# Performance work log

Hardware: AMD Instinct MI355X
Metric: run time of the kernel (lower is better)

## Reference

```python
import jax, jax.numpy as jnp
import numpy as np

B, S, D, H, C = 2, 2048, 1024, 16, 64

def setup_inputs() -> dict:
    key = jax.random.key(0)
    kx, kq, kk, kv, ko = jax.random.split(key, 5)
    scale = 0.02
    return {
        "x": jax.random.normal(kx, (B, S, D), dtype=jnp.float32),
        "Wq": jax.random.normal(kq, (D, H, C), dtype=jnp.float32) * scale,
        "Wk": jax.random.normal(kk, (D, H, C), dtype=jnp.float32) * scale,
        "Wv": jax.random.normal(kv, (D, H, C), dtype=jnp.float32) * scale,
        "Wo": jax.random.normal(ko, (H, C, D), dtype=jnp.float32) * scale,
    }

def reference(x, Wq, Wk, Wv, Wo):
    # project to per-head q/k/v: [B,S,H,C]
    q = jnp.einsum('bqd,dhc->bqhc', x, Wq)
    k = jnp.einsum('bkd,dhc->bkhc', x, Wk)
    v = jnp.einsum('bkd,dhc->bkhc', x, Wv)
    q = q * (C ** -0.5)
    alphas = jnp.einsum('bqhc,bkhc->bhqk', q, k)  # [B,H,S,S]
    weights = jax.nn.softmax(alphas, axis=-1)
    out = jnp.einsum('bhqk,bkhc->bqhc', weights, v)
    return jnp.einsum('bqhc,hcd->bqd', out, Wo)
```

## Files before the change

### kernel.cpp

```cpp
#include <hip/hip_runtime.h>
#include <hip/hip_bf16.h>
#include <stdint.h>
#include <stddef.h>

typedef __bf16 bf16;
typedef __bf16 bf16x4 __attribute__((ext_vector_type(4)));
typedef __bf16 bf16x8 __attribute__((ext_vector_type(8)));
typedef float f32x4 __attribute__((ext_vector_type(4)));

#define DEV __device__ __forceinline__

DEV void async16(const bf16* g, bf16* l) {
    __builtin_amdgcn_global_load_lds(
        (const __attribute__((address_space(1))) void*)g,
        (__attribute__((address_space(3))) void*)l,
        16, 0, 0);
}


__global__ void convert_x(const float* __restrict__ in, bf16* __restrict__ out, int n) {
    int i = (blockIdx.x * blockDim.x + threadIdx.x) * 4;
    if (i >= n) return;
    const float4 v = *(const float4*)(in + i);
    bf16 o4[4] = {(bf16)v.x, (bf16)v.y, (bf16)v.z, (bf16)v.w};
    *(uint2*)(out + i) = *(const uint2*)o4;
}

__global__ void transpose_cvt_all(const float* __restrict__ Wq, const float* __restrict__ Wk,
                                  const float* __restrict__ Wv, const float* __restrict__ Wo,
                                  bf16* __restrict__ WqkvT, bf16* __restrict__ WoT) {
    const float* src;
    bf16* dst;
    float scale = 1.0f;
    switch (blockIdx.z) {
        case 0: src = Wq; dst = WqkvT; scale = 0.125f * 1.4426950408889634f; break;
        case 1: src = Wk; dst = WqkvT + 1024 * 1024; break;
        case 2: src = Wv; dst = WqkvT + 2 * 1024 * 1024; break;
        default: src = Wo; dst = WoT; break;
    }
    __shared__ float t[32][33];
    const int c0 = blockIdx.x * 32, r0 = blockIdx.y * 32;
    const int tx = threadIdx.x & 31, ty = threadIdx.x >> 5;
#pragma unroll
    for (int i = 0; i < 32; i += 8)
        t[ty + i][tx] = src[(size_t)(r0 + ty + i) * 1024 + c0 + tx];
    __syncthreads();
#pragma unroll
    for (int i = 0; i < 32; i += 8)
        dst[(size_t)(c0 + ty + i) * 1024 + r0 + tx] = (bf16)(t[tx][ty + i] * scale);
}

__global__ void transpose_v(const bf16* __restrict__ V, bf16* __restrict__ VT) {
    __shared__ bf16 t[32][33];
    const int c0 = blockIdx.x * 32, r0 = blockIdx.y * 32;
    const int tx = threadIdx.x & 31, ty = threadIdx.x >> 5;
#pragma unroll
    for (int i = 0; i < 32; i += 8)
        t[ty + i][tx] = V[(size_t)(r0 + ty + i) * 3072 + c0 + tx];
    __syncthreads();
#pragma unroll
    for (int i = 0; i < 32; i += 8)
        VT[(size_t)(c0 + ty + i) * 4096 + r0 + tx] = t[tx][ty + i];
}


template <bool OUT_F32>
__global__ __launch_bounds__(256, 3) void gemm_bt(
    const bf16* __restrict__ A, const bf16* __restrict__ BT, void* __restrict__ Cout,
    int M, int N, int K) {
    __shared__ __attribute__((aligned(16))) bf16 As[2 * 128 * 32];
    __shared__ __attribute__((aligned(16))) bf16 Bs[2 * 128 * 32];
    const int tid = threadIdx.x;
    const int wid = tid >> 6;
    const int lane = tid & 63;
    const int quad = lane >> 4;
    const int l16 = lane & 15;
    const int wm = wid >> 1, wn = wid & 1;
    const int m0 = blockIdx.y * 128, n0 = blockIdx.x * 128;

    const int srow = wid * 32 + (lane >> 2);
    const int skcol = (lane & 3) * 8;
    const bf16* ag = A + (size_t)(m0 + srow) * K + skcol;
    const bf16* bg = BT + (size_t)(n0 + srow) * K + skcol;

    f32x4 acc[4][4];
#pragma unroll
    for (int i = 0; i < 4; ++i)
#pragma unroll
        for (int j = 0; j < 4; ++j) acc[i][j] = (f32x4){0.f, 0.f, 0.f, 0.f};

    for (int k0 = 0; k0 < K; k0 += 64) {
#pragma unroll
        for (int p = 0; p < 2; ++p) {
            async16(ag + k0 + p * 32, &As[p * 4096 + (wid * 32) * 32]);
            async16(ag + (size_t)16 * K + k0 + p * 32, &As[p * 4096 + (wid * 32 + 16) * 32]);
            async16(bg + k0 + p * 32, &Bs[p * 4096 + (wid * 32) * 32]);
            async16(bg + (size_t)16 * K + k0 + p * 32, &Bs[p * 4096 + (wid * 32 + 16) * 32]);
        }
        __syncthreads();

#pragma unroll
        for (int ks = 0; ks < 2; ++ks) {
            bf16x8 af[4], bfr[4];
#pragma unroll
            for (int mi = 0; mi < 4; ++mi)
                af[mi] = *(const bf16x8*)&As[ks * 4096 + (wm * 64 + mi * 16 + l16) * 32 + quad * 8];
#pragma unroll
            for (int ni = 0; ni < 4; ++ni)
                bfr[ni] = *(const bf16x8*)&Bs[ks * 4096 + (wn * 64 + ni * 16 + l16) * 32 + quad * 8];
#pragma unroll
            for (int mi = 0; mi < 4; ++mi)
#pragma unroll
                for (int ni = 0; ni < 4; ++ni)
                    acc[mi][ni] = __builtin_amdgcn_mfma_f32_16x16x32_bf16(
                        af[mi], bfr[ni], acc[mi][ni], 0, 0, 0);
        }
        __syncthreads();
    }

    if (OUT_F32) {
        float* C = (float*)Cout;
#pragma unroll
        for (int mi = 0; mi < 4; ++mi)
#pragma unroll
            for (int ni = 0; ni < 4; ++ni)
#pragma unroll
                for (int r = 0; r < 4; ++r)
                    C[(size_t)(m0 + wm * 64 + mi * 16 + quad * 4 + r) * N +
                      (n0 + wn * 64 + ni * 16 + l16)] = acc[mi][ni][r];
    } else {
        bf16* C = (bf16*)Cout;
#pragma unroll
        for (int mi = 0; mi < 4; ++mi)
#pragma unroll
            for (int ni = 0; ni < 4; ++ni)
#pragma unroll
                for (int r = 0; r < 4; ++r)
                    C[(size_t)(m0 + wm * 64 + mi * 16 + quad * 4 + r) * N +
                      (n0 + wn * 64 + ni * 16 + l16)] = (bf16)acc[mi][ni][r];
    }
}


__global__ __launch_bounds__(256, 2) void flash_attn(
    const bf16* __restrict__ QKV, const bf16* __restrict__ VT, bf16* __restrict__ att) {
    __shared__ float Osc[2][32 * 256];
    __shared__ float Lred[4][128];
    __shared__ float Linv[128];

    const int tid = threadIdx.x, wid = tid >> 6, lane = tid & 63;
    const int quad = lane >> 4, l16 = lane & 15;
    const int qt = blockIdx.x;
    const int bh = blockIdx.y;
    const int b = bh >> 4, h = bh & 15;
    const int q0 = qt * 128;

    bf16x8 qf[8][2];
    {
        const bf16* qbase = QKV + (size_t)(b * 2048 + q0 + l16) * 3072 + h * 64 + quad * 8;
#pragma unroll
        for (int mi = 0; mi < 8; ++mi)
#pragma unroll
            for (int ks = 0; ks < 2; ++ks)
                qf[mi][ks] = *(const bf16x8*)(qbase + (size_t)mi * 16 * 3072 + ks * 32);
    }

    const bf16* kbase = QKV + (size_t)(b * 2048 + wid * 16 + l16) * 3072 + 1024 + h * 64 + quad * 8;
    const bf16* vbase = VT + (size_t)(h * 64 + l16) * 4096 + b * 2048 + wid * 16 + quad * 4;

    f32x4 o[8][4];
#pragma unroll
    for (int mi = 0; mi < 8; ++mi)
#pragma unroll
        for (int ct = 0; ct < 4; ++ct) o[mi][ct] = (f32x4){0.f, 0.f, 0.f, 0.f};
    float lsum[8];
#pragma unroll
    for (int mi = 0; mi < 8; ++mi) lsum[mi] = 0.f;

    for (int kc = 0; kc < 32; ++kc) {
        const bf16* kp = kbase + (size_t)kc * 64 * 3072;
        const bf16x8 kf0 = *(const bf16x8*)(kp);
        const bf16x8 kf1 = *(const bf16x8*)(kp + 32);

        const bf16* vp = vbase + kc * 64;
        bf16x8 vf[4];
#pragma unroll
        for (int ct = 0; ct < 4; ++ct) {
            const bf16x4 t = *(const bf16x4*)(vp + (size_t)ct * 16 * 4096);
            vf[ct] = (bf16x8){t[0], t[1], t[2], t[3],
                              (bf16)0.f, (bf16)0.f, (bf16)0.f, (bf16)0.f};
        }

#pragma unroll
        for (int mi = 0; mi < 8; ++mi) {
            f32x4 s = (f32x4){0.f, 0.f, 0.f, 0.f};
            s = __builtin_amdgcn_mfma_f32_16x16x32_bf16(kf0, qf[mi][0], s, 0, 0, 0);
            s = __builtin_amdgcn_mfma_f32_16x16x32_bf16(kf1, qf[mi][1], s, 0, 0, 0);

            const float p0 = __builtin_amdgcn_exp2f(s[0]);
            const float p1 = __builtin_amdgcn_exp2f(s[1]);
            const float p2 = __builtin_amdgcn_exp2f(s[2]);
            const float p3 = __builtin_amdgcn_exp2f(s[3]);
            lsum[mi] += (p0 + p1) + (p2 + p3);
            const bf16x8 pf = (bf16x8){(bf16)p0, (bf16)p1, (bf16)p2, (bf16)p3,
                                       (bf16)0.f, (bf16)0.f, (bf16)0.f, (bf16)0.f};
#pragma unroll
            for (int ct = 0; ct < 4; ++ct)
                o[mi][ct] = __builtin_amdgcn_mfma_f32_16x16x32_bf16(pf, vf[ct], o[mi][ct], 0, 0, 0);
        }
    }

#pragma unroll
    for (int mi = 0; mi < 8; ++mi) {
        lsum[mi] += __shfl_xor(lsum[mi], 16);
        lsum[mi] += __shfl_xor(lsum[mi], 32);
    }
    if (quad == 0) {
#pragma unroll
        for (int mi = 0; mi < 8; ++mi) Lred[wid][mi * 16 + l16] = lsum[mi];
    }
    if (wid >= 2) {
        float* dst = &Osc[wid - 2][0];
#pragma unroll
        for (int mi = 0; mi < 8; ++mi)
#pragma unroll
            for (int ct = 0; ct < 4; ++ct)
                *(f32x4*)(dst + (mi * 4 + ct) * 256 + lane * 4) = o[mi][ct];
    }
    __syncthreads();

    if (tid < 128) {
        const float l = Lred[0][tid] + Lred[1][tid] + Lred[2][tid] + Lred[3][tid];
        Linv[tid] = 1.0f / l;
    }
    if (wid < 2) {
        const float* src = &Osc[wid][0];
#pragma unroll
        for (int mi = 0; mi < 8; ++mi)
#pragma unroll
            for (int ct = 0; ct < 4; ++ct)
                o[mi][ct] += *(const f32x4*)(src + (mi * 4 + ct) * 256 + lane * 4);
    }
    __syncthreads();

    if (wid == 1) {
        float* dst = &Osc[0][0];
#pragma unroll
        for (int mi = 0; mi < 8; ++mi)
#pragma unroll
            for (int ct = 0; ct < 4; ++ct)
                *(f32x4*)(dst + (mi * 4 + ct) * 256 + lane * 4) = o[mi][ct];
    }
    __syncthreads();

    if (wid == 0) {
        const float* src = &Osc[0][0];
#pragma unroll
        for (int mi = 0; mi < 8; ++mi)
#pragma unroll
            for (int ct = 0; ct < 4; ++ct)
                o[mi][ct] += *(const f32x4*)(src + (mi * 4 + ct) * 256 + lane * 4);
#pragma unroll
        for (int mi = 0; mi < 8; ++mi)
#pragma unroll
            for (int r = 0; r < 4; ++r) {
                const float inv = Linv[mi * 16 + quad * 4 + r];
                bf16* orow = att + (size_t)(b * 2048 + q0 + mi * 16 + quad * 4 + r) * 1024 + h * 64 + l16;
#pragma unroll
                for (int ct = 0; ct < 4; ++ct)
                    orow[ct * 16] = (bf16)(o[mi][ct][r] * inv);
            }
    }
}


extern "C" void kernel_launch(void* const* d_in, const int* in_sizes, int n_in,
                              void* d_out, int out_size, void* d_ws, size_t ws_size,
                              hipStream_t stream) {
    (void)in_sizes; (void)n_in; (void)out_size; (void)ws_size;
    const float* x  = (const float*)d_in[0];
    const float* Wq = (const float*)d_in[1];
    const float* Wk = (const float*)d_in[2];
    const float* Wv = (const float*)d_in[3];
    const float* Wo = (const float*)d_in[4];

    char* ws = (char*)d_ws;
    bf16* xb    = (bf16*)(ws);
    bf16* att   = xb;
    bf16* WqkvT = (bf16*)(ws + (size_t)8  * 1024 * 1024);
    bf16* WoT   = (bf16*)(ws + (size_t)14 * 1024 * 1024);
    bf16* QKV   = (bf16*)(ws + (size_t)16 * 1024 * 1024);
    bf16* VT    = (bf16*)(ws + (size_t)40 * 1024 * 1024);

    const int n_x = 2 * 2048 * 1024;
    convert_x<<<n_x / (256 * 4), 256, 0, stream>>>(x, xb, n_x);

    transpose_cvt_all<<<dim3(32, 32, 4), 256, 0, stream>>>(Wq, Wk, Wv, Wo, WqkvT, WoT);

    gemm_bt<false><<<dim3(3072 / 128, 4096 / 128), 256, 0, stream>>>(
        xb, WqkvT, QKV, 4096, 3072, 1024);

    transpose_v<<<dim3(32, 128), 256, 0, stream>>>(QKV + 2048, VT);

    flash_attn<<<dim3(16, 32), 256, 0, stream>>>(QKV, VT, att);

    gemm_bt<true><<<dim3(1024 / 128, 4096 / 128), 256, 0, stream>>>(
        att, WoT, (float*)d_out, 4096, 1024, 1024);
}
```

Measured before the change: 199.4 us.

## Stage K/V tiles in LDS with register prefetch and 2x2 warp split

```diff
diff --git a/kernel.cpp b/kernel.cpp
--- a/kernel.cpp
+++ b/kernel.cpp
@@ -144,128 +144,145 @@
 
 __global__ __launch_bounds__(256, 2) void flash_attn(
     const bf16* __restrict__ QKV, const bf16* __restrict__ VT, bf16* __restrict__ att) {
-    __shared__ float Osc[2][32 * 256];
-    __shared__ float Lred[4][128];
-    __shared__ float Linv[128];
+    constexpr int LDK = 72;
+    constexpr int LDV = 136;
+    __shared__ __attribute__((aligned(16))) char smem[36864];
+    bf16* Ks = (bf16*)smem;
+    bf16* Vs = (bf16*)(smem + 18432);
+    float* Osc = (float*)smem;
+    float* Lred = (float*)(smem + 32768);
 
     const int tid = threadIdx.x, wid = tid >> 6, lane = tid & 63;
     const int quad = lane >> 4, l16 = lane & 15;
-    const int qt = blockIdx.x;
-    const int bh = blockIdx.y;
+    const int qh = wid >> 1, kh = wid & 1;
+    const int qt = blockIdx.x, bh = blockIdx.y;
     const int b = bh >> 4, h = bh & 15;
     const int q0 = qt * 128;
 
-    bf16x8 qf[8][2];
+    bf16x8 qf[4][2];
     {
-        const bf16* qbase = QKV + (size_t)(b * 2048 + q0 + l16) * 3072 + h * 64 + quad * 8;
-#pragma unroll
-        for (int mi = 0; mi < 8; ++mi)
+        const bf16* qbase = QKV + (size_t)(b * 2048 + q0 + qh * 64 + l16) * 3072 + h * 64 + quad * 8;
+#pragma unroll
+        for (int mi = 0; mi < 4; ++mi)
 #pragma unroll
             for (int ks = 0; ks < 2; ++ks)
                 qf[mi][ks] = *(const bf16x8*)(qbase + (size_t)mi * 16 * 3072 + ks * 32);
     }
 
-    const bf16* kbase = QKV + (size_t)(b * 2048 + wid * 16 + l16) * 3072 + 1024 + h * 64 + quad * 8;
-    const bf16* vbase = VT + (size_t)(h * 64 + l16) * 4096 + b * 2048 + wid * 16 + quad * 4;
-
-    f32x4 o[8][4];
-#pragma unroll
-    for (int mi = 0; mi < 8; ++mi)
+    const int krow = tid >> 3, kcol = (tid & 7) * 8;
+    const int vrow = tid >> 4, vcol = (tid & 15) * 8;
+    const bf16* kg = QKV + (size_t)(b * 2048 + krow) * 3072 + 1024 + h * 64 + kcol;
+    const bf16* vg = VT + (size_t)(h * 64 + vrow) * 4096 + b * 2048 + vcol;
+
+    bf16x8 kr[4], vr[4];
+#pragma unroll
+    for (int p = 0; p < 4; ++p) {
+        kr[p] = *(const bf16x8*)(kg + (size_t)(32 * p) * 3072);
+        vr[p] = *(const bf16x8*)(vg + (size_t)(16 * p) * 4096);
+    }
+
+    f32x4 o[4][4];
+    float lsum[4];
+#pragma unroll
+    for (int mi = 0; mi < 4; ++mi) {
+        lsum[mi] = 0.f;
 #pragma unroll
         for (int ct = 0; ct < 4; ++ct) o[mi][ct] = (f32x4){0.f, 0.f, 0.f, 0.f};
-    float lsum[8];
-#pragma unroll
-    for (int mi = 0; mi < 8; ++mi) lsum[mi] = 0.f;
-
-    for (int kc = 0; kc < 32; ++kc) {
-        const bf16* kp = kbase + (size_t)kc * 64 * 3072;
-        const bf16x8 kf0 = *(const bf16x8*)(kp);
-        const bf16x8 kf1 = *(const bf16x8*)(kp + 32);
-
-        const bf16* vp = vbase + kc * 64;
-        bf16x8 vf[4];
-#pragma unroll
-        for (int ct = 0; ct < 4; ++ct) {
-            const bf16x4 t = *(const bf16x4*)(vp + (size_t)ct * 16 * 4096);
-            vf[ct] = (bf16x8){t[0], t[1], t[2], t[3],
-                              (bf16)0.f, (bf16)0.f, (bf16)0.f, (bf16)0.f};
-        }
-
-#pragma unroll
-        for (int mi = 0; mi < 8; ++mi) {
-            f32x4 s = (f32x4){0.f, 0.f, 0.f, 0.f};
-            s = __builtin_amdgcn_mfma_f32_16x16x32_bf16(kf0, qf[mi][0], s, 0, 0, 0);
-            s = __builtin_amdgcn_mfma_f32_16x16x32_bf16(kf1, qf[mi][1], s, 0, 0, 0);
-
-            const float p0 = __builtin_amdgcn_exp2f(s[0]);
-            const float p1 = __builtin_amdgcn_exp2f(s[1]);
-            const float p2 = __builtin_amdgcn_exp2f(s[2]);
-            const float p3 = __builtin_amdgcn_exp2f(s[3]);
-            lsum[mi] += (p0 + p1) + (p2 + p3);
-            const bf16x8 pf = (bf16x8){(bf16)p0, (bf16)p1, (bf16)p2, (bf16)p3,
-                                       (bf16)0.f, (bf16)0.f, (bf16)0.f, (bf16)0.f};
-#pragma unroll
-            for (int ct = 0; ct < 4; ++ct)
-                o[mi][ct] = __builtin_amdgcn_mfma_f32_16x16x32_bf16(pf, vf[ct], o[mi][ct], 0, 0, 0);
-        }
-    }
-
-#pragma unroll
-    for (int mi = 0; mi < 8; ++mi) {
+    }
+
+    for (int it = 0; it < 16; ++it) {
+#pragma unroll
+        for (int p = 0; p < 4; ++p) {
+            *(bf16x8*)&Ks[(32 * p + krow) * LDK + kcol] = kr[p];
+            *(bf16x8*)&Vs[(16 * p + vrow) * LDV + vcol] = vr[p];
+        }
+        __syncthreads();
+
+        if (it < 15) {
+            const size_t ko = (size_t)(it + 1) * 128;
+#pragma unroll
+            for (int p = 0; p < 4; ++p) {
+                kr[p] = *(const bf16x8*)(kg + (ko + 32 * p) * 3072);
+                vr[p] = *(const bf16x8*)(vg + (size_t)(16 * p) * 4096 + ko);
+            }
+        }
+
+#pragma unroll
+        for (int pr = 0; pr < 2; ++pr) {
+            const int kb = kh * 64 + pr * 32;
+            const bf16x8 kfA0 = *(const bf16x8*)&Ks[(kb + l16) * LDK + quad * 8];
+            const bf16x8 kfA1 = *(const bf16x8*)&Ks[(kb + l16) * LDK + 32 + quad * 8];
+            const bf16x8 kfB0 = *(const bf16x8*)&Ks[(kb + 16 + l16) * LDK + quad * 8];
+            const bf16x8 kfB1 = *(const bf16x8*)&Ks[(kb + 16 + l16) * LDK + 32 + quad * 8];
+            bf16x8 vf[4];
+#pragma unroll
+            for (int ct = 0; ct < 4; ++ct) {
+                const bf16x4 lo = *(const bf16x4*)&Vs[(ct * 16 + l16) * LDV + kb + quad * 4];
+                const bf16x4 hi = *(const bf16x4*)&Vs[(ct * 16 + l16) * LDV + kb + 16 + quad * 4];
+                vf[ct] = (bf16x8){lo[0], lo[1], lo[2], lo[3], hi[0], hi[1], hi[2], hi[3]};
+            }
+#pragma unroll
+            for (int mi = 0; mi < 4; ++mi) {
+                f32x4 sA = (f32x4){0.f, 0.f, 0.f, 0.f};
+                f32x4 sB = (f32x4){0.f, 0.f, 0.f, 0.f};
+                sA = __builtin_amdgcn_mfma_f32_16x16x32_bf16(kfA0, qf[mi][0], sA, 0, 0, 0);
+                sA = __builtin_amdgcn_mfma_f32_16x16x32_bf16(kfA1, qf[mi][1], sA, 0, 0, 0);
+                sB = __builtin_amdgcn_mfma_f32_16x16x32_bf16(kfB0, qf[mi][0], sB, 0, 0, 0);
+                sB = __builtin_amdgcn_mfma_f32_16x16x32_bf16(kfB1, qf[mi][1], sB, 0, 0, 0);
+
+                const float pa0 = __builtin_amdgcn_exp2f(sA[0]);
+                const float pa1 = __builtin_amdgcn_exp2f(sA[1]);
+                const float pa2 = __builtin_amdgcn_exp2f(sA[2]);
+                const float pa3 = __builtin_amdgcn_exp2f(sA[3]);
+                const float pb0 = __builtin_amdgcn_exp2f(sB[0]);
+                const float pb1 = __builtin_amdgcn_exp2f(sB[1]);
+                const float pb2 = __builtin_amdgcn_exp2f(sB[2]);
+                const float pb3 = __builtin_amdgcn_exp2f(sB[3]);
+                lsum[mi] += ((pa0 + pa1) + (pa2 + pa3)) + ((pb0 + pb1) + (pb2 + pb3));
+                const bf16x8 pf = (bf16x8){(bf16)pa0, (bf16)pa1, (bf16)pa2, (bf16)pa3,
+                                           (bf16)pb0, (bf16)pb1, (bf16)pb2, (bf16)pb3};
+#pragma unroll
+                for (int ct = 0; ct < 4; ++ct)
+                    o[mi][ct] = __builtin_amdgcn_mfma_f32_16x16x32_bf16(pf, vf[ct], o[mi][ct], 0, 0, 0);
+            }
+        }
+        __syncthreads();
+    }
+
+#pragma unroll
+    for (int mi = 0; mi < 4; ++mi) {
         lsum[mi] += __shfl_xor(lsum[mi], 16);
         lsum[mi] += __shfl_xor(lsum[mi], 32);
     }
     if (quad == 0) {
 #pragma unroll
-        for (int mi = 0; mi < 8; ++mi) Lred[wid][mi * 16 + l16] = lsum[mi];
-    }
-    if (wid >= 2) {
-        float* dst = &Osc[wid - 2][0];
-#pragma unroll
-        for (int mi = 0; mi < 8; ++mi)
+        for (int mi = 0; mi < 4; ++mi) Lred[wid * 64 + mi * 16 + l16] = lsum[mi];
+    }
+    if (kh == 1) {
+        float* dst = Osc + qh * 4096;
+#pragma unroll
+        for (int mi = 0; mi < 4; ++mi)
 #pragma unroll
             for (int ct = 0; ct < 4; ++ct)
                 *(f32x4*)(dst + (mi * 4 + ct) * 256 + lane * 4) = o[mi][ct];
     }
     __syncthreads();
 
-    if (tid < 128) {
-        const float l = Lred[0][tid] + Lred[1][tid] + Lred[2][tid] + Lred[3][tid];
-        Linv[tid] = 1.0f / l;
-    }
-    if (wid < 2) {
-        const float* src = &Osc[wid][0];
-#pragma unroll
-        for (int mi = 0; mi < 8; ++mi)
+    if (kh == 0) {
+        const float* src = Osc + qh * 4096;
+#pragma unroll
+        for (int mi = 0; mi < 4; ++mi)
 #pragma unroll
             for (int ct = 0; ct < 4; ++ct)
                 o[mi][ct] += *(const f32x4*)(src + (mi * 4 + ct) * 256 + lane * 4);
-    }
-    __syncthreads();
-
-    if (wid == 1) {
-        float* dst = &Osc[0][0];
-#pragma unroll
-        for (int mi = 0; mi < 8; ++mi)
-#pragma unroll
-            for (int ct = 0; ct < 4; ++ct)
-                *(f32x4*)(dst + (mi * 4 + ct) * 256 + lane * 4) = o[mi][ct];
-    }
-    __syncthreads();
-
-    if (wid == 0) {
-        const float* src = &Osc[0][0];
-#pragma unroll
-        for (int mi = 0; mi < 8; ++mi)
-#pragma unroll
-            for (int ct = 0; ct < 4; ++ct)
-                o[mi][ct] += *(const f32x4*)(src + (mi * 4 + ct) * 256 + lane * 4);
-#pragma unroll
-        for (int mi = 0; mi < 8; ++mi)
+#pragma unroll
+        for (int mi = 0; mi < 4; ++mi)
 #pragma unroll
             for (int r = 0; r < 4; ++r) {
-                const float inv = Linv[mi * 16 + quad * 4 + r];
-                bf16* orow = att + (size_t)(b * 2048 + q0 + mi * 16 + quad * 4 + r) * 1024 + h * 64 + l16;
+                const int qrow = mi * 16 + quad * 4 + r;
+                const float l = Lred[(qh * 2) * 64 + qrow] + Lred[(qh * 2 + 1) * 64 + qrow];
+                const float inv = 1.0f / l;
+                bf16* orow = att + (size_t)(b * 2048 + q0 + qh * 64 + qrow) * 1024 + h * 64 + l16;
 #pragma unroll
                 for (int ct = 0; ct < 4; ++ct)
                     orow[ct * 16] = (bf16)(o[mi][ct][r] * inv);
```

After: 188.2 us. 5.6% less time.
